# Performance work log

Measured on AMD Instinct MI355X. Metric: run time of the kernel, lower is better.

Reference implementation:

```python
import jax, jax.numpy as jnp
import numpy as np

EPS = 1e-12


def _pchip_slopes(y, x):
    """PCHIP (Fritsch-Carlson) slopes. y: (S, K), x: (K) -> (S, K)."""
    K = y.shape[-1]
    if K < 2:
        return jnp.zeros_like(y)
    h = x[1:] - x[:-1]                              # (K-1,)
    delta = (y[..., 1:] - y[..., :-1]) / (h + EPS)  # (S, K-1)
    if K == 2:
        return jnp.broadcast_to(delta[..., :1], y.shape).astype(y.dtype)
    # interior slopes: weighted harmonic mean where secants agree in sign
    delta_prev = delta[..., :-1]
    delta_next = delta[..., 1:]
    same_sign = delta_prev * delta_next > 0
    h_prev = h[:-1]
    h_next = h[1:]
    w1 = 2.0 * h_next + h_prev
    w2 = h_next + 2.0 * h_prev
    denom = w1 / (delta_prev + EPS) + w2 / (delta_next + EPS)
    d_int = (w1 + w2) / (denom + EPS)
    d_mid = jnp.where(same_sign, d_int, jnp.zeros_like(d_int))  # (S, K-2)
    # left endpoint (one-sided, shape-limited)
    h0, h1 = h[0], h[1]
    delta0 = delta[..., 0]
    delta1 = delta[..., 1]
    d0 = ((2.0 * h0 + h1) * delta0 - h0 * delta1) / (h0 + h1 + EPS)
    d0 = jnp.where(jnp.sign(d0) != jnp.sign(delta0), jnp.zeros_like(d0), d0)
    d0 = jnp.where((jnp.sign(delta0) != jnp.sign(delta1)) & (jnp.abs(d0) > 3.0 * jnp.abs(delta0)), 3.0 * delta0, d0)
    # right endpoint
    hn1, hn2 = h[-1], h[-2]
    deltan1 = delta[..., -1]
    deltan2 = delta[..., -2]
    dn = ((2.0 * hn1 + hn2) * deltan1 - hn1 * deltan2) / (hn1 + hn2 + EPS)
    dn = jnp.where(jnp.sign(dn) != jnp.sign(deltan1), jnp.zeros_like(dn), dn)
    dn = jnp.where((jnp.sign(deltan1) != jnp.sign(deltan2)) & (jnp.abs(dn) > 3.0 * jnp.abs(deltan1)), 3.0 * deltan1, dn)
    return jnp.concatenate([d0[..., None], d_mid, dn[..., None]], axis=-1)


def setup_inputs() -> dict:
    key = jax.random.key(0)
    k1, k2 = jax.random.split(key)
    B, S, K = 4096, 4096, 64
    x_min, x_max = -3.0, 3.0
    xq = jax.random.normal(k1, (B, S), dtype=jnp.float32) * 2.0  # some queries outside domain
    coeffs = jax.random.normal(k2, (S, K), dtype=jnp.float32)
    knots = jnp.linspace(x_min, x_max, K, dtype=jnp.float32)
    return {"xq": xq, "coeffs": coeffs, "knots": knots}


def reference(xq, coeffs, knots):
    y = coeffs                                   # (S, K)
    d = _pchip_slopes(y, knots)                  # (S, K)
    K = knots.shape[0]
    x0_dom = knots[0]
    x1_dom = knots[-1]
    below = xq < x0_dom
    above = xq > x1_dom
    xq_c = jnp.clip(xq, x0_dom, x1_dom)
    idx = jnp.searchsorted(knots, xq_c) - 1      # (B, S) interval index
    idx = jnp.clip(idx, 0, K - 2)
    x0 = knots[idx]
    x1 = knots[idx + 1]
    h = x1 - x0 + EPS
    t = (xq_c - x0) / h
    t2 = t * t
    t3 = t2 * t
    h00 = 2.0 * t3 - 3.0 * t2 + 1.0
    h10 = t3 - 2.0 * t2 + t
    h01 = -2.0 * t3 + 3.0 * t2
    h11 = t3 - t2
    s_idx = jnp.arange(y.shape[0])[None, :]      # (1, S) spline index
    y0 = y[s_idx, idx]
    y1 = y[s_idx, idx + 1]
    d0 = d[s_idx, idx]
    d1 = d[s_idx, idx + 1]
    interp = h00 * y0 + h10 * h * d0 + h01 * y1 + h11 * h * d1
    out = jnp.where(below, y[None, :, 0] + d[None, :, 0] * (xq - x0_dom), interp)
    out = jnp.where(above, y[None, :, -1] + d[None, :, -1] * (xq - x1_dom), out)
    return out
```

## Files before the change

### kernel.cpp

```cpp
#include <hip/hip_runtime.h>

#define EPSF 1e-12f
#define STILE 64
#define KK 64
#define LSTR 65
#define PLANE (STILE * LSTR)
#define BLK 512
#define UNROLL 8

__device__ __forceinline__ float sgnf(float x) {
    return (x > 0.f) ? 1.f : ((x < 0.f) ? -1.f : 0.f);
}

__global__ __launch_bounds__(BLK, 4) void pchip_fused2(
    const float* __restrict__ xq,
    const float* __restrict__ coeffs,
    const float* __restrict__ knots,
    float* __restrict__ out,
    int S, int b_chunk)
{
    __shared__ float pl[4 * PLANE];
    __shared__ float skn[KK];

    int tid = threadIdx.x;
    int s0 = blockIdx.x * STILE;
    int b0 = blockIdx.y * b_chunk;

    float* p0 = pl;
    float* p1 = pl + PLANE;
    float* p2 = pl + 2 * PLANE;
    float* p3 = pl + 3 * PLANE;

    if (tid < KK) skn[tid] = knots[tid];
#pragma unroll
    for (int i = 0; i < (STILE * KK) / BLK; i++) {
        int p = tid + i * BLK;
        int sl = p >> 6, k = p & 63;
        p0[sl * LSTR + k] = coeffs[(size_t)(s0 + sl) * KK + k];
    }
    __syncthreads();
#pragma unroll
    for (int i = 0; i < (STILE * KK) / BLK; i++) {
        int p = tid + i * BLK;
        int sl = p >> 6, k = p & 63;
        if (k < KK - 1) {
            float h = skn[k + 1] - skn[k];
            p3[sl * LSTR + k] = (p0[sl * LSTR + k + 1] - p0[sl * LSTR + k]) / (h + EPSF);
        }
    }
    __syncthreads();
    float dreg[(STILE * KK) / BLK];
#pragma unroll
    for (int i = 0; i < (STILE * KK) / BLK; i++) {
        int p = tid + i * BLK;
        int sl = p >> 6, k = p & 63;
        const float* del = p3 + sl * LSTR;
        float d;
        if (k == 0) {
            float h0 = skn[1] - skn[0], h1 = skn[2] - skn[1];
            float de0 = del[0], de1 = del[1];
            d = ((2.f * h0 + h1) * de0 - h0 * de1) / (h0 + h1 + EPSF);
            if (sgnf(d) != sgnf(de0)) d = 0.f;
            if ((sgnf(de0) != sgnf(de1)) && (fabsf(d) > 3.f * fabsf(de0))) d = 3.f * de0;
        } else if (k == KK - 1) {
            float hn1 = skn[KK - 1] - skn[KK - 2], hn2 = skn[KK - 2] - skn[KK - 3];
            float dn1 = del[KK - 2], dn2 = del[KK - 3];
            d = ((2.f * hn1 + hn2) * dn1 - hn1 * dn2) / (hn1 + hn2 + EPSF);
            if (sgnf(d) != sgnf(dn1)) d = 0.f;
            if ((sgnf(dn1) != sgnf(dn2)) && (fabsf(d) > 3.f * fabsf(dn1))) d = 3.f * dn1;
        } else {
            float dprev = del[k - 1], dnext = del[k];
            float hp = skn[k] - skn[k - 1], hn = skn[k + 1] - skn[k];
            bool same = dprev * dnext > 0.f;
            float w1 = 2.f * hn + hp;
            float w2 = hn + 2.f * hp;
            float denom = w1 / (dprev + EPSF) + w2 / (dnext + EPSF);
            float dint = (w1 + w2) / (denom + EPSF);
            d = same ? dint : 0.f;
        }
        dreg[i] = d;
    }
    __syncthreads();
#pragma unroll
    for (int i = 0; i < (STILE * KK) / BLK; i++) {
        int p = tid + i * BLK;
        int sl = p >> 6, k = p & 63;
        p2[sl * LSTR + k] = dreg[i];
    }
    __syncthreads();
    float c1r[(STILE * KK) / BLK], c2r[(STILE * KK) / BLK], c3r[(STILE * KK) / BLK];
#pragma unroll
    for (int i = 0; i < (STILE * KK) / BLK; i++) {
        int p = tid + i * BLK;
        int sl = p >> 6, k = p & 63;
        int kc = min(k, KK - 2);
        int ib = sl * LSTR + kc;
        float y0 = p0[ib], y1 = p0[ib + 1];
        float d0 = p2[ib], d1 = p2[ib + 1];
        float h = skn[kc + 1] - skn[kc] + EPSF;
        c1r[i] = h * d0;
        c2r[i] = 3.f * (y1 - y0) - h * (2.f * d0 + d1);
        c3r[i] = 2.f * (y0 - y1) + h * (d0 + d1);
    }
    __syncthreads();
#pragma unroll
    for (int i = 0; i < (STILE * KK) / BLK; i++) {
        int p = tid + i * BLK;
        int sl = p >> 6, k = p & 63;
        if (k < KK - 1) {
            int ib = sl * LSTR + k;
            p1[ib] = c1r[i];
            p2[ib] = c2r[i];
            p3[ib] = c3r[i];
        }
    }
    __syncthreads();

    float x0d = skn[0], x1d = skn[KK - 1];
    float invh = (float)(KK - 1) / (x1d - x0d);
    float af = invh, bf = -x0d * invh;
    int wave = tid >> 6, lane = tid & 63;
    const float* q0 = p0 + lane * LSTR;
    const float* q1 = p1 + lane * LSTR;
    const float* q2 = p2 + lane * LSTR;
    const float* q3 = p3 + lane * LSTR;

    int rows_per_wave = b_chunk >> 3;
    size_t off0 = (size_t)(b0 + wave * rows_per_wave) * S + s0 + lane;
    for (int ii = 0; ii < rows_per_wave; ii += UNROLL) {
        float xv[UNROLL];
#pragma unroll
        for (int j = 0; j < UNROLL; j++) xv[j] = xq[off0 + (size_t)j * S];
        float rv[UNROLL];
#pragma unroll
        for (int j = 0; j < UNROLL; j++) {
            float x = xv[j];
            float tf = fmaf(x, af, bf);
            float tcf = fminf(fmaxf(tf, 0.f), (float)(KK - 1));
            int idx = min((int)tcf, KK - 2);
            float t = tcf - (float)idx;
            float c0 = q0[idx], c1 = q1[idx], c2 = q2[idx], c3 = q3[idx];
            float P = fmaf(fmaf(fmaf(c3, t, c2), t, c1), t, c0);
            float w = fmaf(fmaf(t, 2.f, t), c3, c2 + c2);
            float Pp = fmaf(t, w, c1);
            float ext = tf - tcf;
            rv[j] = fmaf(Pp, ext, P);
        }
#pragma unroll
        for (int j = 0; j < UNROLL; j++) out[off0 + (size_t)j * S] = rv[j];
        off0 += (size_t)UNROLL * S;
    }
}

extern "C" void kernel_launch(void* const* d_in, const int* in_sizes, int n_in,
                              void* d_out, int out_size, void* d_ws, size_t ws_size,
                              hipStream_t stream) {
    const float* xq     = (const float*)d_in[0];
    const float* coeffs = (const float*)d_in[1];
    const float* knots  = (const float*)d_in[2];
    float* out = (float*)d_out;

    int K = in_sizes[2];
    int S = in_sizes[1] / K;
    int N = in_sizes[0];
    int B = N / S;

    int n_btiles = 8;
    int b_chunk = B / n_btiles;
    dim3 grid(S / STILE, n_btiles);
    pchip_fused2<<<grid, BLK, 0, stream>>>(xq, coeffs, knots, out, S, b_chunk);
}
```

Baseline: 123.9 us.

## Interleave spline coefficients as float4 in LDS and halve spline tile

Stores the four cubic coefficients per interval interleaved as one float4 in shared memory, so each query does a single 128-bit LDS read instead of four scalar reads. The spline tile shrinks from 64 to 32, and each wave now covers two batch rows with 32 splines each, which halves LDS per block and raises the occupancy hint to 8 blocks. Global loads become two 128-byte segments per wave instead of one 256-byte segment. The grid doubles, so coefficient setup is repeated across more blocks.

New measurement: 124.2 us. No clear change (+0.2%).

```diff
diff --git a/kernel.cpp b/kernel.cpp
--- a/kernel.cpp
+++ b/kernel.cpp
@@ -1,60 +1,58 @@
 #include <hip/hip_runtime.h>
 
 #define EPSF 1e-12f
-#define STILE 64
+#define STILE 32
 #define KK 64
-#define LSTR 65
-#define PLANE (STILE * LSTR)
+#define QSTR 65
+#define ROWF (QSTR * 4)
 #define BLK 512
+#define ENT ((STILE * KK) / BLK)
 #define UNROLL 8
 
 __device__ __forceinline__ float sgnf(float x) {
     return (x > 0.f) ? 1.f : ((x < 0.f) ? -1.f : 0.f);
 }
 
-__global__ __launch_bounds__(BLK, 4) void pchip_fused2(
+__global__ __launch_bounds__(BLK, 8) void pchip_fused3(
     const float* __restrict__ xq,
     const float* __restrict__ coeffs,
     const float* __restrict__ knots,
     float* __restrict__ out,
     int S, int b_chunk)
 {
-    __shared__ float pl[4 * PLANE];
+    __shared__ float4 quads[STILE * QSTR];
     __shared__ float skn[KK];
+    float* fp = (float*)quads;
 
     int tid = threadIdx.x;
     int s0 = blockIdx.x * STILE;
     int b0 = blockIdx.y * b_chunk;
 
-    float* p0 = pl;
-    float* p1 = pl + PLANE;
-    float* p2 = pl + 2 * PLANE;
-    float* p3 = pl + 3 * PLANE;
-
     if (tid < KK) skn[tid] = knots[tid];
 #pragma unroll
-    for (int i = 0; i < (STILE * KK) / BLK; i++) {
+    for (int i = 0; i < ENT; i++) {
         int p = tid + i * BLK;
         int sl = p >> 6, k = p & 63;
-        p0[sl * LSTR + k] = coeffs[(size_t)(s0 + sl) * KK + k];
+        fp[sl * ROWF + k] = coeffs[(size_t)(s0 + sl) * KK + k];
     }
     __syncthreads();
 #pragma unroll
-    for (int i = 0; i < (STILE * KK) / BLK; i++) {
+    for (int i = 0; i < ENT; i++) {
         int p = tid + i * BLK;
         int sl = p >> 6, k = p & 63;
         if (k < KK - 1) {
             float h = skn[k + 1] - skn[k];
-            p3[sl * LSTR + k] = (p0[sl * LSTR + k + 1] - p0[sl * LSTR + k]) / (h + EPSF);
+            fp[sl * ROWF + 64 + k] =
+                (fp[sl * ROWF + k + 1] - fp[sl * ROWF + k]) / (h + EPSF);
         }
     }
     __syncthreads();
-    float dreg[(STILE * KK) / BLK];
+    float dreg[ENT];
 #pragma unroll
-    for (int i = 0; i < (STILE * KK) / BLK; i++) {
+    for (int i = 0; i < ENT; i++) {
         int p = tid + i * BLK;
         int sl = p >> 6, k = p & 63;
-        const float* del = p3 + sl * LSTR;
+        const float* del = fp + sl * ROWF + 64;
         float d;
         if (k == 0) {
             float h0 = skn[1] - skn[0], h1 = skn[2] - skn[1];
@@ -82,37 +80,33 @@
     }
     __syncthreads();
 #pragma unroll
-    for (int i = 0; i < (STILE * KK) / BLK; i++) {
+    for (int i = 0; i < ENT; i++) {
         int p = tid + i * BLK;
         int sl = p >> 6, k = p & 63;
-        p2[sl * LSTR + k] = dreg[i];
+        fp[sl * ROWF + 128 + k] = dreg[i];
     }
     __syncthreads();
-    float c1r[(STILE * KK) / BLK], c2r[(STILE * KK) / BLK], c3r[(STILE * KK) / BLK];
+    float4 qreg[ENT];
 #pragma unroll
-    for (int i = 0; i < (STILE * KK) / BLK; i++) {
+    for (int i = 0; i < ENT; i++) {
         int p = tid + i * BLK;
         int sl = p >> 6, k = p & 63;
         int kc = min(k, KK - 2);
-        int ib = sl * LSTR + kc;
-        float y0 = p0[ib], y1 = p0[ib + 1];
-        float d0 = p2[ib], d1 = p2[ib + 1];
+        const float* row = fp + sl * ROWF;
+        float y0 = row[kc], y1 = row[kc + 1];
+        float d0 = row[128 + kc], d1 = row[128 + kc + 1];
         float h = skn[kc + 1] - skn[kc] + EPSF;
-        c1r[i] = h * d0;
-        c2r[i] = 3.f * (y1 - y0) - h * (2.f * d0 + d1);
-        c3r[i] = 2.f * (y0 - y1) + h * (d0 + d1);
+        qreg[i] = make_float4(y0,
+                              h * d0,
+                              3.f * (y1 - y0) - h * (2.f * d0 + d1),
+                              2.f * (y0 - y1) + h * (d0 + d1));
     }
     __syncthreads();
 #pragma unroll
-    for (int i = 0; i < (STILE * KK) / BLK; i++) {
+    for (int i = 0; i < ENT; i++) {
         int p = tid + i * BLK;
         int sl = p >> 6, k = p & 63;
-        if (k < KK - 1) {
-            int ib = sl * LSTR + k;
-            p1[ib] = c1r[i];
-            p2[ib] = c2r[i];
-            p3[ib] = c3r[i];
-        }
+        if (k < KK - 1) quads[sl * QSTR + k] = qreg[i];
     }
     __syncthreads();
 
@@ -120,17 +114,16 @@
     float invh = (float)(KK - 1) / (x1d - x0d);
     float af = invh, bf = -x0d * invh;
     int wave = tid >> 6, lane = tid & 63;
-    const float* q0 = p0 + lane * LSTR;
-    const float* q1 = p1 + lane * LSTR;
-    const float* q2 = p2 + lane * LSTR;
-    const float* q3 = p3 + lane * LSTR;
+    int srow = lane & 31;
+    int bpar = lane >> 5;
+    const float4* qrow = quads + srow * QSTR;
 
-    int rows_per_wave = b_chunk >> 3;
-    size_t off0 = (size_t)(b0 + wave * rows_per_wave) * S + s0 + lane;
-    for (int ii = 0; ii < rows_per_wave; ii += UNROLL) {
+    int pairs_per_wave = b_chunk >> 4;
+    size_t off0 = (size_t)(b0 + wave * pairs_per_wave * 2 + bpar) * S + s0 + srow;
+    for (int ii = 0; ii < pairs_per_wave; ii += UNROLL) {
         float xv[UNROLL];
 #pragma unroll
-        for (int j = 0; j < UNROLL; j++) xv[j] = xq[off0 + (size_t)j * S];
+        for (int j = 0; j < UNROLL; j++) xv[j] = xq[off0 + (size_t)(2 * j) * S];
         float rv[UNROLL];
 #pragma unroll
         for (int j = 0; j < UNROLL; j++) {
@@ -139,16 +132,15 @@
             float tcf = fminf(fmaxf(tf, 0.f), (float)(KK - 1));
             int idx = min((int)tcf, KK - 2);
             float t = tcf - (float)idx;
-            float c0 = q0[idx], c1 = q1[idx], c2 = q2[idx], c3 = q3[idx];
-            float P = fmaf(fmaf(fmaf(c3, t, c2), t, c1), t, c0);
-            float w = fmaf(fmaf(t, 2.f, t), c3, c2 + c2);
-            float Pp = fmaf(t, w, c1);
-            float ext = tf - tcf;
-            rv[j] = fmaf(Pp, ext, P);
+            float4 c = qrow[idx];
+            float P = fmaf(fmaf(fmaf(c.w, t, c.z), t, c.y), t, c.x);
+            float w = fmaf(fmaf(t, 2.f, t), c.w, c.z + c.z);
+            float Pp = fmaf(t, w, c.y);
+            rv[j] = fmaf(Pp, tf - tcf, P);
         }
 #pragma unroll
-        for (int j = 0; j < UNROLL; j++) out[off0 + (size_t)j * S] = rv[j];
-        off0 += (size_t)UNROLL * S;
+        for (int j = 0; j < UNROLL; j++) out[off0 + (size_t)(2 * j) * S] = rv[j];
+        off0 += (size_t)(2 * UNROLL) * S;
     }
 }
 
@@ -168,5 +160,5 @@
     int n_btiles = 8;
     int b_chunk = B / n_btiles;
     dim3 grid(S / STILE, n_btiles);
-    pchip_fused2<<<grid, BLK, 0, stream>>>(xq, coeffs, knots, out, S, b_chunk);
+    pchip_fused3<<<grid, BLK, 0, stream>>>(xq, coeffs, knots, out, S, b_chunk);
 }
```
